# Kernel tuning notes

Measured on AMD Instinct MI355X. Metric: run time of the kernel, lower is better.

Reference implementation:

```python
import jax, jax.numpy as jnp
import numpy as np

N = 1 << 20        # number of query points
L_HIDDEN = 6       # hidden (64->64) layers, i.e. params[1:-1]
NEG_SLOPE = 0.2    # nn.LeakyReLU(0.2)

# NOTE: nn.Dropout(0.5) is treated in eval mode (identity), the standard
# convention for deterministic correctness baselines.

def _lrelu(x):
    return jnp.where(x >= 0, x, NEG_SLOPE * x)


def setup_inputs() -> dict:
    key = jax.random.key(0)
    ks = jax.random.split(key, 11)
    return {
        "points": jax.random.normal(ks[0], (N, 3), jnp.float32),
        "w0": jax.random.normal(ks[1], (3, 64), jnp.float32),
        "s0": jax.random.normal(ks[2], (64,), jnp.float32),
        "b0": jax.random.normal(ks[3], (64,), jnp.float32),
        "wh": jax.random.normal(ks[4], (L_HIDDEN, 64, 64), jnp.float32),
        "sh": jax.random.normal(ks[5], (L_HIDDEN, 64), jnp.float32),
        "bh": jax.random.normal(ks[6], (L_HIDDEN, 64), jnp.float32),
        "wo": jax.random.normal(ks[7], (64, 1), jnp.float32),
        "so": jax.random.normal(ks[8], (), jnp.float32),
        "bo": jax.random.normal(ks[9], (), jnp.float32),
    }


def reference(points, w0, s0, b0, wh, sh, bh, wo, so, bo):
    # first layer: [N,3] @ [3,64] * scale + bias -> leakyrelu
    x = _lrelu(jnp.matmul(points, w0) * s0 + b0)
    # hidden layers: small static loop over structurally distinct param sets
    for i in range(L_HIDDEN):
        x = _lrelu(jnp.matmul(x, wh[i]) * sh[i] + bh[i])
    # output layer: [N,64] @ [64,1] * scalar + scalar (no activation)
    return jnp.matmul(x, wo) * so + bo
```

## Files before the change

### kernel.cpp

```cpp
#include <hip/hip_runtime.h>


typedef _Float16 half8 __attribute__((ext_vector_type(8)));
typedef _Float16 half2v __attribute__((ext_vector_type(2)));
typedef float floatx16 __attribute__((ext_vector_type(16)));

#define N_HID 6
#define OFF_A 0
#define OFF_B 49152
#define OFF_C 51200
#define OFF_D 52992
#define IMG_BYTES 53248
#define SETUP_TOTAL (24576 + 1024 + 448 + 64)

__global__ __launch_bounds__(256) void setup_weights(
    const float* __restrict__ w0, const float* __restrict__ s0, const float* __restrict__ b0,
    const float* __restrict__ wh, const float* __restrict__ sh, const float* __restrict__ bh,
    const float* __restrict__ wo, const float* __restrict__ so,
    unsigned char* __restrict__ ws)
{
    int i = blockIdx.x * 256 + threadIdx.x;
    if (i < 24576) {
        int j = i & 7, lane = (i >> 3) & 63, s = (i >> 9) & 3, t = (i >> 11) & 1, l = i >> 12;
        int m = 32 * t + (lane & 31);
        int h = lane >> 5;
        int feat = 16 * s + 8 * (j >> 2) + 4 * h + (j & 3);
        ((_Float16*)(ws + OFF_A))[i] = (_Float16)(wh[(l * 64 + feat) * 64 + m] * sh[l * 64 + m]);
    } else if (i < 24576 + 1024) {
        int i2 = i - 24576;
        int j = i2 & 7, lane = (i2 >> 3) & 63, t = i2 >> 9;
        int m = 32 * t + (lane & 31);
        int k = 8 * (lane >> 5) + j;
        float v = (k < 3) ? w0[k * 64 + m] * s0[m] * 0.015625f : 0.f;
        ((_Float16*)(ws + OFF_B))[i2] = (_Float16)v;
    } else if (i < 24576 + 1024 + 448) {
        int i2 = i - 24576 - 1024;
        int r = i2 & 15, t = (i2 >> 4) & 1, h = (i2 >> 5) & 1, l = i2 >> 6;
        int feat = 32 * t + (r & 3) + 8 * ((r >> 2) & 3) + 4 * h;
        float bv = (l == 0) ? b0[feat] : bh[(l - 1) * 64 + feat];
        ((float*)(ws + OFF_C))[i2] = bv * 0.015625f;
    } else if (i < SETUP_TOTAL) {
        int i2 = i - 24576 - 1024 - 448;
        int r = i2 & 15, t = (i2 >> 4) & 1, h = i2 >> 5;
        int feat = 32 * t + (r & 3) + 8 * ((r >> 2) & 3) + 4 * h;
        ((float*)(ws + OFF_D))[i2] = wo[feat] * so[0] * 64.f;
    }
}

union FragU { int i[4]; half8 v; };

static __device__ __forceinline__ int pkrtz(float a, float b) {
    auto hh = __builtin_amdgcn_cvt_pkrtz(a, b);
    int r;
    __builtin_memcpy(&r, &hh, 4);
    return r;
}

static __device__ __forceinline__ int lrelu2(int v) {
    half2v u;
    __builtin_memcpy(&u, &v, 4);
    half2v w = u * (_Float16)0.2f;
    half2v r = __builtin_elementwise_max(u, w);
    int o;
    __builtin_memcpy(&o, &r, 4);
    return o;
}

static __device__ __forceinline__ floatx16 mfma16(half8 a, half8 b, floatx16 c) {
    return __builtin_amdgcn_mfma_f32_32x32x16_f16(a, b, c, 0, 0, 0);
}

__global__ __launch_bounds__(512, 4) void mlp_mfma(
    const float* __restrict__ points,
    const unsigned char* __restrict__ ws,
    const float* __restrict__ bo,
    float* __restrict__ out, int n)
{
    __shared__ __align__(16) unsigned char lds[IMG_BYTES];

    {
        const uint4* src = (const uint4*)ws;
        uint4* dst = (uint4*)lds;
#pragma unroll
        for (int i = 0; i < 6; ++i) {
            int idx = threadIdx.x + 512 * i;
            dst[idx] = src[idx];
        }
        if (threadIdx.x < 256) {
            int idx = 3072 + threadIdx.x;
            dst[idx] = src[idx];
        }
    }
    __syncthreads();

    const int lane = threadIdx.x & 63;
    const int wv = threadIdx.x >> 6;
    const int p = lane & 31;
    const int h = lane >> 5;
    const int base = (blockIdx.x * 8 + wv) * 64;
    const int pt0 = base + p, pt1 = base + 32 + p;
    const int pl0 = min(pt0, n - 1), pl1 = min(pt1, n - 1);

    const half8* Wf = (const half8*)(lds + OFF_A);
    const half8* A0 = (const half8*)(lds + OFF_B);
    const floatx16* biasC = (const floatx16*)(lds + OFF_C);
    const floatx16* woC = (const floatx16*)(lds + OFF_D);

    floatx16 acc[2][2];
    int fr[2][16];

    {
        FragU bu0, bu1;
        bu0.i[0] = bu0.i[1] = bu0.i[2] = bu0.i[3] = 0;
        bu1 = bu0;
        if (h == 0) {
            bu0.v[0] = (_Float16)points[3 * pl0 + 0];
            bu0.v[1] = (_Float16)points[3 * pl0 + 1];
            bu0.v[2] = (_Float16)points[3 * pl0 + 2];
            bu1.v[0] = (_Float16)points[3 * pl1 + 0];
            bu1.v[1] = (_Float16)points[3 * pl1 + 1];
            bu1.v[2] = (_Float16)points[3 * pl1 + 2];
        }
        floatx16 c0 = biasC[h * 2 + 0];
        floatx16 c1 = biasC[h * 2 + 1];
        half8 a0 = A0[lane], a1 = A0[64 + lane];
        acc[0][0] = mfma16(a0, bu0.v, c0);
        acc[0][1] = mfma16(a1, bu0.v, c1);
        acc[1][0] = mfma16(a0, bu1.v, c0);
        acc[1][1] = mfma16(a1, bu1.v, c1);
    }

    auto packfr = [&]() {
#pragma unroll
        for (int nt = 0; nt < 2; ++nt)
#pragma unroll
            for (int t = 0; t < 2; ++t)
#pragma unroll
                for (int rp = 0; rp < 8; ++rp) {
                    int v = pkrtz(acc[nt][t][2 * rp], acc[nt][t][2 * rp + 1]);
                    fr[nt][8 * t + 2 * (rp >> 1) + (rp & 1)] = lrelu2(v);
                }
    };
    packfr();

    for (int l = 0; l < N_HID; ++l) {
        floatx16 c0 = biasC[((l + 1) * 2 + h) * 2 + 0];
        floatx16 c1 = biasC[((l + 1) * 2 + h) * 2 + 1];
        const half8* wl = Wf + l * 512 + lane;
        acc[0][0] = c0; acc[0][1] = c1; acc[1][0] = c0; acc[1][1] = c1;
#pragma unroll
        for (int s = 0; s < 4; ++s) {
            half8 wt0 = wl[s * 64];
            half8 wt1 = wl[256 + s * 64];
            FragU f0, f1;
#pragma unroll
            for (int c = 0; c < 4; ++c) { f0.i[c] = fr[0][4 * s + c]; f1.i[c] = fr[1][4 * s + c]; }
            acc[0][0] = mfma16(wt0, f0.v, acc[0][0]);
            acc[0][1] = mfma16(wt1, f0.v, acc[0][1]);
            acc[1][0] = mfma16(wt0, f1.v, acc[1][0]);
            acc[1][1] = mfma16(wt1, f1.v, acc[1][1]);
        }
        if (l < N_HID - 1) packfr();
    }

    {
        floatx16 wo0 = woC[h * 2 + 0];
        floatx16 wo1 = woC[h * 2 + 1];
        float part0 = 0.f, part1 = 0.f;
#pragma unroll
        for (int r = 0; r < 16; ++r) {
            float u;
            u = acc[0][0][r]; part0 = fmaf(fmaxf(u, 0.2f * u), wo0[r], part0);
            u = acc[0][1][r]; part0 = fmaf(fmaxf(u, 0.2f * u), wo1[r], part0);
            u = acc[1][0][r]; part1 = fmaf(fmaxf(u, 0.2f * u), wo0[r], part1);
            u = acc[1][1][r]; part1 = fmaf(fmaxf(u, 0.2f * u), wo1[r], part1);
        }
        part0 += __shfl_xor(part0, 32);
        part1 += __shfl_xor(part1, 32);
        const float bov = bo[0];
        if (h == 0) {
            if (pt0 < n) out[pt0] = part0 + bov;
            if (pt1 < n) out[pt1] = part1 + bov;
        }
    }
}

extern "C" void kernel_launch(void* const* d_in, const int* in_sizes, int n_in,
                              void* d_out, int out_size, void* d_ws, size_t ws_size,
                              hipStream_t stream) {
    const float* points = (const float*)d_in[0];
    const float* w0     = (const float*)d_in[1];
    const float* s0     = (const float*)d_in[2];
    const float* b0     = (const float*)d_in[3];
    const float* wh     = (const float*)d_in[4];
    const float* sh     = (const float*)d_in[5];
    const float* bh     = (const float*)d_in[6];
    const float* wo     = (const float*)d_in[7];
    const float* so     = (const float*)d_in[8];
    const float* bo     = (const float*)d_in[9];

    const int n = in_sizes[0] / 3;

    setup_weights<<<(SETUP_TOTAL + 255) / 256, 256, 0, stream>>>(
        w0, s0, b0, wh, sh, bh, wo, so, (unsigned char*)d_ws);

    const int grid = (n + 511) / 512;
    mlp_mfma<<<grid, 512, 0, stream>>>(
        points, (const unsigned char*)d_ws, bo, (float*)d_out, n);
}
```

Measured before the change: 128.9 us.

## Compute output layer with MFMA and add setprio around MFMA chains

The final 64->1 projection moves from a per-lane scalar FMA reduction plus a cross-half shuffle onto MFMA instructions, using an fp16 weight image broadcast into a fragment layout. The last hidden layer's activations are packed to fp16 the same way as earlier layers. MFMA sequences are wrapped in s_setprio to favour issue among waves, and fragments are kept as int4 vectors to avoid union repacking. The cost is a larger LDS image (less occupancy headroom), wasted MFMA columns for the single output, and an extra fp16 rounding step on the output-layer weights and activations.

New measurement: 128.2 us. Within noise of the previous version (-0.5%).

```diff
diff --git a/kernel.cpp b/kernel.cpp
--- a/kernel.cpp
+++ b/kernel.cpp
@@ -4,14 +4,15 @@
 typedef _Float16 half8 __attribute__((ext_vector_type(8)));
 typedef _Float16 half2v __attribute__((ext_vector_type(2)));
 typedef float floatx16 __attribute__((ext_vector_type(16)));
+typedef int int4v __attribute__((ext_vector_type(4)));
 
 #define N_HID 6
 #define OFF_A 0
 #define OFF_B 49152
 #define OFF_C 51200
 #define OFF_D 52992
-#define IMG_BYTES 53248
-#define SETUP_TOTAL (24576 + 1024 + 448 + 64)
+#define IMG_BYTES 57088
+#define SETUP_TOTAL (24576 + 1024 + 448 + 2048)
 
 __global__ __launch_bounds__(256) void setup_weights(
     const float* __restrict__ w0, const float* __restrict__ s0, const float* __restrict__ b0,
@@ -40,14 +41,13 @@
         float bv = (l == 0) ? b0[feat] : bh[(l - 1) * 64 + feat];
         ((float*)(ws + OFF_C))[i2] = bv * 0.015625f;
     } else if (i < SETUP_TOTAL) {
-        int i2 = i - 24576 - 1024 - 448;
-        int r = i2 & 15, t = (i2 >> 4) & 1, h = i2 >> 5;
-        int feat = 32 * t + (r & 3) + 8 * ((r >> 2) & 3) + 4 * h;
-        ((float*)(ws + OFF_D))[i2] = wo[feat] * so[0] * 64.f;
-    }
-}
-
-union FragU { int i[4]; half8 v; };
+        int i2 = i - (24576 + 1024 + 448);
+        int j = i2 & 7, lane = (i2 >> 3) & 63, s = i2 >> 9;
+        int h = lane >> 5;
+        int feat = 16 * s + 8 * (j >> 2) + 4 * h + (j & 3);
+        ((_Float16*)(ws + OFF_D))[i2] = (_Float16)(wo[feat] * so[0] * 64.f);
+    }
+}
 
 static __device__ __forceinline__ int pkrtz(float a, float b) {
     auto hh = __builtin_amdgcn_cvt_pkrtz(a, b);
@@ -66,6 +66,12 @@
     return o;
 }
 
+static __device__ __forceinline__ half8 as_h8(int4v v) {
+    half8 r;
+    __builtin_memcpy(&r, &v, 16);
+    return r;
+}
+
 static __device__ __forceinline__ floatx16 mfma16(half8 a, half8 b, floatx16 c) {
     return __builtin_amdgcn_mfma_f32_32x32x16_f16(a, b, c, 0, 0, 0);
 }
@@ -86,7 +92,7 @@
             int idx = threadIdx.x + 512 * i;
             dst[idx] = src[idx];
         }
-        if (threadIdx.x < 256) {
+        if (threadIdx.x < 496) {
             int idx = 3072 + threadIdx.x;
             dst[idx] = src[idx];
         }
@@ -104,30 +110,29 @@
     const half8* Wf = (const half8*)(lds + OFF_A);
     const half8* A0 = (const half8*)(lds + OFF_B);
     const floatx16* biasC = (const floatx16*)(lds + OFF_C);
-    const floatx16* woC = (const floatx16*)(lds + OFF_D);
+    const half8* woA = (const half8*)(lds + OFF_D);
 
     floatx16 acc[2][2];
-    int fr[2][16];
+    int4v frv[2][4];
 
     {
-        FragU bu0, bu1;
-        bu0.i[0] = bu0.i[1] = bu0.i[2] = bu0.i[3] = 0;
-        bu1 = bu0;
+        int4v z4 = {0, 0, 0, 0};
+        int4v b0v = z4, b1v = z4;
         if (h == 0) {
-            bu0.v[0] = (_Float16)points[3 * pl0 + 0];
-            bu0.v[1] = (_Float16)points[3 * pl0 + 1];
-            bu0.v[2] = (_Float16)points[3 * pl0 + 2];
-            bu1.v[0] = (_Float16)points[3 * pl1 + 0];
-            bu1.v[1] = (_Float16)points[3 * pl1 + 1];
-            bu1.v[2] = (_Float16)points[3 * pl1 + 2];
+            b0v[0] = pkrtz(points[3 * pl0 + 0], points[3 * pl0 + 1]);
+            b0v[1] = pkrtz(points[3 * pl0 + 2], 0.f);
+            b1v[0] = pkrtz(points[3 * pl1 + 0], points[3 * pl1 + 1]);
+            b1v[1] = pkrtz(points[3 * pl1 + 2], 0.f);
         }
         floatx16 c0 = biasC[h * 2 + 0];
         floatx16 c1 = biasC[h * 2 + 1];
         half8 a0 = A0[lane], a1 = A0[64 + lane];
-        acc[0][0] = mfma16(a0, bu0.v, c0);
-        acc[0][1] = mfma16(a1, bu0.v, c1);
-        acc[1][0] = mfma16(a0, bu1.v, c0);
-        acc[1][1] = mfma16(a1, bu1.v, c1);
+        __builtin_amdgcn_s_setprio(1);
+        acc[0][0] = mfma16(a0, as_h8(b0v), c0);
+        acc[0][1] = mfma16(a1, as_h8(b0v), c1);
+        acc[1][0] = mfma16(a0, as_h8(b1v), c0);
+        acc[1][1] = mfma16(a1, as_h8(b1v), c1);
+        __builtin_amdgcn_s_setprio(0);
     }
 
     auto packfr = [&]() {
@@ -138,49 +143,55 @@
 #pragma unroll
                 for (int rp = 0; rp < 8; ++rp) {
                     int v = pkrtz(acc[nt][t][2 * rp], acc[nt][t][2 * rp + 1]);
-                    fr[nt][8 * t + 2 * (rp >> 1) + (rp & 1)] = lrelu2(v);
+                    int idx = 8 * t + rp;
+                    frv[nt][idx >> 2][idx & 3] = lrelu2(v);
                 }
     };
     packfr();
 
     for (int l = 0; l < N_HID; ++l) {
-        floatx16 c0 = biasC[((l + 1) * 2 + h) * 2 + 0];
-        floatx16 c1 = biasC[((l + 1) * 2 + h) * 2 + 1];
+        const floatx16 c0 = biasC[((l + 1) * 2 + h) * 2 + 0];
+        const floatx16 c1 = biasC[((l + 1) * 2 + h) * 2 + 1];
         const half8* wl = Wf + l * 512 + lane;
-        acc[0][0] = c0; acc[0][1] = c1; acc[1][0] = c0; acc[1][1] = c1;
+        __builtin_amdgcn_s_setprio(1);
+        {
+            half8 w0 = wl[0], w1 = wl[256];
+            half8 f0 = as_h8(frv[0][0]), f1 = as_h8(frv[1][0]);
+            acc[0][0] = mfma16(w0, f0, c0);
+            acc[0][1] = mfma16(w1, f0, c1);
+            acc[1][0] = mfma16(w0, f1, c0);
+            acc[1][1] = mfma16(w1, f1, c1);
+        }
+#pragma unroll
+        for (int s = 1; s < 4; ++s) {
+            half8 w0 = wl[s * 64], w1 = wl[256 + s * 64];
+            half8 f0 = as_h8(frv[0][s]), f1 = as_h8(frv[1][s]);
+            acc[0][0] = mfma16(w0, f0, acc[0][0]);
+            acc[0][1] = mfma16(w1, f0, acc[0][1]);
+            acc[1][0] = mfma16(w0, f1, acc[1][0]);
+            acc[1][1] = mfma16(w1, f1, acc[1][1]);
+        }
+        __builtin_amdgcn_s_setprio(0);
+        packfr();
+    }
+
+    {
+        floatx16 z;
+#pragma unroll
+        for (int r = 0; r < 16; ++r) z[r] = 0.f;
+        floatx16 o0 = z, o1 = z;
+        __builtin_amdgcn_s_setprio(1);
 #pragma unroll
         for (int s = 0; s < 4; ++s) {
-            half8 wt0 = wl[s * 64];
-            half8 wt1 = wl[256 + s * 64];
-            FragU f0, f1;
-#pragma unroll
-            for (int c = 0; c < 4; ++c) { f0.i[c] = fr[0][4 * s + c]; f1.i[c] = fr[1][4 * s + c]; }
-            acc[0][0] = mfma16(wt0, f0.v, acc[0][0]);
-            acc[0][1] = mfma16(wt1, f0.v, acc[0][1]);
-            acc[1][0] = mfma16(wt0, f1.v, acc[1][0]);
-            acc[1][1] = mfma16(wt1, f1.v, acc[1][1]);
-        }
-        if (l < N_HID - 1) packfr();
-    }
-
-    {
-        floatx16 wo0 = woC[h * 2 + 0];
-        floatx16 wo1 = woC[h * 2 + 1];
-        float part0 = 0.f, part1 = 0.f;
-#pragma unroll
-        for (int r = 0; r < 16; ++r) {
-            float u;
-            u = acc[0][0][r]; part0 = fmaf(fmaxf(u, 0.2f * u), wo0[r], part0);
-            u = acc[0][1][r]; part0 = fmaf(fmaxf(u, 0.2f * u), wo1[r], part0);
-            u = acc[1][0][r]; part1 = fmaf(fmaxf(u, 0.2f * u), wo0[r], part1);
-            u = acc[1][1][r]; part1 = fmaf(fmaxf(u, 0.2f * u), wo1[r], part1);
-        }
-        part0 += __shfl_xor(part0, 32);
-        part1 += __shfl_xor(part1, 32);
+            half8 w = woA[s * 64 + lane];
+            o0 = mfma16(w, as_h8(frv[0][s]), o0);
+            o1 = mfma16(w, as_h8(frv[1][s]), o1);
+        }
+        __builtin_amdgcn_s_setprio(0);
         const float bov = bo[0];
         if (h == 0) {
-            if (pt0 < n) out[pt0] = part0 + bov;
-            if (pt1 < n) out[pt1] = part1 + bov;
+            if (pt0 < n) out[pt0] = o0[0] + bov;
+            if (pt1 < n) out[pt1] = o1[0] + bov;
         }
     }
 }
```

## Halve per-wave point tile to 32 and add MFMA priority hints

Applied to the files above, without the earlier changes.

Each wave now processes 32 points instead of 64, which halves the accumulator and fragment registers and doubles the grid. Each block therefore stages the weight image into LDS for half as many points, and each weight fragment read from LDS feeds only two MFMAs instead of four. The MFMA chains are wrapped in s_setprio to favour matrix issue, and the first accumulation is seeded directly from the bias rather than by a separate copy. The aim is higher occupancy and latency hiding, paid for with more LDS weight traffic and more block-setup overhead per point.

Measured after the change: 136.9 us. +6.2%, slower.

```diff
diff --git a/kernel.cpp b/kernel.cpp
--- a/kernel.cpp
+++ b/kernel.cpp
@@ -4,6 +4,7 @@
 typedef _Float16 half8 __attribute__((ext_vector_type(8)));
 typedef _Float16 half2v __attribute__((ext_vector_type(2)));
 typedef float floatx16 __attribute__((ext_vector_type(16)));
+typedef int int4v __attribute__((ext_vector_type(4)));
 
 #define N_HID 6
 #define OFF_A 0
@@ -47,8 +48,6 @@
     }
 }
 
-union FragU { int i[4]; half8 v; };
-
 static __device__ __forceinline__ int pkrtz(float a, float b) {
     auto hh = __builtin_amdgcn_cvt_pkrtz(a, b);
     int r;
@@ -64,6 +63,12 @@
     int o;
     __builtin_memcpy(&o, &r, 4);
     return o;
+}
+
+static __device__ __forceinline__ half8 as_h8(int4v v) {
+    half8 r;
+    __builtin_memcpy(&r, &v, 16);
+    return r;
 }
 
 static __device__ __forceinline__ floatx16 mfma16(half8 a, half8 b, floatx16 c) {
@@ -97,91 +102,71 @@
     const int wv = threadIdx.x >> 6;
     const int p = lane & 31;
     const int h = lane >> 5;
-    const int base = (blockIdx.x * 8 + wv) * 64;
-    const int pt0 = base + p, pt1 = base + 32 + p;
-    const int pl0 = min(pt0, n - 1), pl1 = min(pt1, n - 1);
+    const int pt = (blockIdx.x * 8 + wv) * 32 + p;
+    const int pl = min(pt, n - 1);
 
     const half8* Wf = (const half8*)(lds + OFF_A);
     const half8* A0 = (const half8*)(lds + OFF_B);
     const floatx16* biasC = (const floatx16*)(lds + OFF_C);
     const floatx16* woC = (const floatx16*)(lds + OFF_D);
 
-    floatx16 acc[2][2];
-    int fr[2][16];
+    floatx16 acc[2];
+    int4v frv[4];
 
     {
-        FragU bu0, bu1;
-        bu0.i[0] = bu0.i[1] = bu0.i[2] = bu0.i[3] = 0;
-        bu1 = bu0;
+        int4v bv = {0, 0, 0, 0};
         if (h == 0) {
-            bu0.v[0] = (_Float16)points[3 * pl0 + 0];
-            bu0.v[1] = (_Float16)points[3 * pl0 + 1];
-            bu0.v[2] = (_Float16)points[3 * pl0 + 2];
-            bu1.v[0] = (_Float16)points[3 * pl1 + 0];
-            bu1.v[1] = (_Float16)points[3 * pl1 + 1];
-            bu1.v[2] = (_Float16)points[3 * pl1 + 2];
+            bv[0] = pkrtz(points[3 * pl + 0], points[3 * pl + 1]);
+            bv[1] = pkrtz(points[3 * pl + 2], 0.f);
         }
         floatx16 c0 = biasC[h * 2 + 0];
         floatx16 c1 = biasC[h * 2 + 1];
-        half8 a0 = A0[lane], a1 = A0[64 + lane];
-        acc[0][0] = mfma16(a0, bu0.v, c0);
-        acc[0][1] = mfma16(a1, bu0.v, c1);
-        acc[1][0] = mfma16(a0, bu1.v, c0);
-        acc[1][1] = mfma16(a1, bu1.v, c1);
+        __builtin_amdgcn_s_setprio(1);
+        acc[0] = mfma16(A0[lane], as_h8(bv), c0);
+        acc[1] = mfma16(A0[64 + lane], as_h8(bv), c1);
+        __builtin_amdgcn_s_setprio(0);
     }
 
     auto packfr = [&]() {
 #pragma unroll
-        for (int nt = 0; nt < 2; ++nt)
+        for (int t = 0; t < 2; ++t)
 #pragma unroll
-            for (int t = 0; t < 2; ++t)
-#pragma unroll
-                for (int rp = 0; rp < 8; ++rp) {
-                    int v = pkrtz(acc[nt][t][2 * rp], acc[nt][t][2 * rp + 1]);
-                    fr[nt][8 * t + 2 * (rp >> 1) + (rp & 1)] = lrelu2(v);
-                }
+            for (int rp = 0; rp < 8; ++rp) {
+                int v = pkrtz(acc[t][2 * rp], acc[t][2 * rp + 1]);
+                int idx = 8 * t + rp;
+                frv[idx >> 2][idx & 3] = lrelu2(v);
+            }
     };
     packfr();
 
     for (int l = 0; l < N_HID; ++l) {
-        floatx16 c0 = biasC[((l + 1) * 2 + h) * 2 + 0];
-        floatx16 c1 = biasC[((l + 1) * 2 + h) * 2 + 1];
+        const floatx16 c0 = biasC[((l + 1) * 2 + h) * 2 + 0];
+        const floatx16 c1 = biasC[((l + 1) * 2 + h) * 2 + 1];
         const half8* wl = Wf + l * 512 + lane;
-        acc[0][0] = c0; acc[0][1] = c1; acc[1][0] = c0; acc[1][1] = c1;
+        __builtin_amdgcn_s_setprio(1);
+        acc[0] = mfma16(wl[0],   as_h8(frv[0]), c0);
+        acc[1] = mfma16(wl[256], as_h8(frv[0]), c1);
 #pragma unroll
-        for (int s = 0; s < 4; ++s) {
-            half8 wt0 = wl[s * 64];
-            half8 wt1 = wl[256 + s * 64];
-            FragU f0, f1;
-#pragma unroll
-            for (int c = 0; c < 4; ++c) { f0.i[c] = fr[0][4 * s + c]; f1.i[c] = fr[1][4 * s + c]; }
-            acc[0][0] = mfma16(wt0, f0.v, acc[0][0]);
-            acc[0][1] = mfma16(wt1, f0.v, acc[0][1]);
-            acc[1][0] = mfma16(wt0, f1.v, acc[1][0]);
-            acc[1][1] = mfma16(wt1, f1.v, acc[1][1]);
+        for (int s = 1; s < 4; ++s) {
+            acc[0] = mfma16(wl[s * 64],       as_h8(frv[s]), acc[0]);
+            acc[1] = mfma16(wl[256 + s * 64], as_h8(frv[s]), acc[1]);
         }
+        __builtin_amdgcn_s_setprio(0);
         if (l < N_HID - 1) packfr();
     }
 
     {
         floatx16 wo0 = woC[h * 2 + 0];
         floatx16 wo1 = woC[h * 2 + 1];
-        float part0 = 0.f, part1 = 0.f;
+        float part = 0.f;
 #pragma unroll
         for (int r = 0; r < 16; ++r) {
             float u;
-            u = acc[0][0][r]; part0 = fmaf(fmaxf(u, 0.2f * u), wo0[r], part0);
-            u = acc[0][1][r]; part0 = fmaf(fmaxf(u, 0.2f * u), wo1[r], part0);
-            u = acc[1][0][r]; part1 = fmaf(fmaxf(u, 0.2f * u), wo0[r], part1);
-            u = acc[1][1][r]; part1 = fmaf(fmaxf(u, 0.2f * u), wo1[r], part1);
+            u = acc[0][r]; part = fmaf(fmaxf(u, 0.2f * u), wo0[r], part);
+            u = acc[1][r]; part = fmaf(fmaxf(u, 0.2f * u), wo1[r], part);
         }
-        part0 += __shfl_xor(part0, 32);
-        part1 += __shfl_xor(part1, 32);
-        const float bov = bo[0];
-        if (h == 0) {
-            if (pt0 < n) out[pt0] = part0 + bov;
-            if (pt1 < n) out[pt1] = part1 + bov;
-        }
+        part += __shfl_xor(part, 32);
+        if (h == 0 && pt < n) out[pt] = part + bo[0];
     }
 }
 
@@ -204,7 +189,7 @@
     setup_weights<<<(SETUP_TOTAL + 255) / 256, 256, 0, stream>>>(
         w0, s0, b0, wh, sh, bh, wo, so, (unsigned char*)d_ws);
 
-    const int grid = (n + 511) / 512;
+    const int grid = (n + 255) / 256;
     mlp_mfma<<<grid, 512, 0, stream>>>(
         points, (const unsigned char*)d_ws, bo, (float*)d_out, n);
 }
```
